# Kernel optimization log

Measured on AMD Instinct MI355X. Metric: run time of the kernel, lower is better.

Reference implementation:

```python
import jax, jax.numpy as jnp
import numpy as np

NEG_BIG = -1e9


def setup_inputs() -> dict:
    key = jax.random.key(0)
    ks = jax.random.split(key, 6)
    B, Tq, Tv, D, A = 4, 256, 1024, 512, 128
    inputs = jax.random.normal(ks[0], (B, Tv, D), dtype=jnp.float32)
    context = jax.random.normal(ks[1], (B, Tq, D), dtype=jnp.float32)
    mask = jnp.ones((B, Tv), dtype=jnp.int32)  # 1 = valid position
    scale = 1.0 / np.sqrt(D)
    Wk = jax.random.normal(ks[2], (D, A), dtype=jnp.float32) * scale
    bk = jnp.zeros((A,), dtype=jnp.float32)
    Wq = jax.random.normal(ks[3], (D, A), dtype=jnp.float32) * scale
    bq = jnp.zeros((A,), dtype=jnp.float32)
    attn_v = jax.random.normal(ks[4], (A,), dtype=jnp.float32) * (1.0 / np.sqrt(A))
    return {"inputs": inputs, "context": context, "mask": mask,
            "Wk": Wk, "bk": bk, "Wq": Wq, "bq": bq, "attn_v": attn_v}


def reference(inputs, context, mask, Wk, bk, Wq, bq, attn_v):
    # inputs: [B,Tv,D] (keys/values), context: [B,Tq,D] (queries)
    k = jnp.einsum('bvd,da->bva', inputs, Wk) + bk        # [B,Tv,A]
    q = jnp.einsum('bqd,da->bqa', context, Wq) + bq       # [B,Tq,A]
    # additive (Bahdanau) score: sum_a v_a * tanh(q + k)
    t = jnp.tanh(q[:, :, None, :] + k[:, None, :, :])     # [B,Tq,Tv,A]
    scores = jnp.einsum('bqva,a->bqv', t, attn_v)         # [B,Tq,Tv]
    neg = (1.0 - mask.astype(jnp.float32))[:, None, :] * NEG_BIG
    scores = scores + neg
    attn = jax.nn.softmax(scores, axis=-1)                # [B,Tq,Tv]
    return jnp.einsum('bqv,bvd->bqd', attn, inputs)       # [B,Tq,D]
```

## Files before the change

### kernel.cpp

```cpp
#include <hip/hip_runtime.h>
#include <math.h>

#define B   4
#define TQ  256
#define TV  1024
#define D   512
#define A   128

#define LOG2E     1.4426950408889634f
#define TWO_LOG2E 2.8853900817779268f
#define NEG_BIG_F (-1e9f)

#define QBLK (B * TQ / 8)
#define KBLK (B * TV / 8)

__global__ __launch_bounds__(256, 4) void proj_exp_kernel(
    const float* __restrict__ ctx, const float* __restrict__ inp,
    const float* __restrict__ Wq, const float* __restrict__ bq,
    const float* __restrict__ Wk, const float* __restrict__ bk,
    float* __restrict__ Eq, float* __restrict__ EkT) {
  __shared__ float xs[8][D];
  __shared__ float ps[8][4][A];
  __shared__ float es[A][9];

  bool isQ = blockIdx.x < QBLK;
  const float* X; const float* W; const float* bias; int r0;
  if (isQ) { X = ctx; W = Wq; bias = bq; r0 = blockIdx.x * 8; }
  else     { X = inp; W = Wk; bias = bk; r0 = (blockIdx.x - QBLK) * 8; }

  int tid = threadIdx.x;

  {
    const float4* Xv = (const float4*)(X + (size_t)r0 * D);
    float4* xsv = (float4*)&xs[0][0];
    for (int i = tid; i < 8 * D / 4; i += 256) xsv[i] = Xv[i];
  }
  __syncthreads();

  int aq = (tid & 31) * 4;
  int h  = tid >> 5;
  float4 acc[8];
#pragma unroll
  for (int j = 0; j < 8; ++j) acc[j] = make_float4(0.f, 0.f, 0.f, 0.f);

  int dbase = h * 64;
#pragma unroll 2
  for (int dd = 0; dd < 64; dd += 4) {
    int d = dbase + dd;
    float4 w0 = *(const float4*)(W + (size_t)(d + 0) * A + aq);
    float4 w1 = *(const float4*)(W + (size_t)(d + 1) * A + aq);
    float4 w2 = *(const float4*)(W + (size_t)(d + 2) * A + aq);
    float4 w3 = *(const float4*)(W + (size_t)(d + 3) * A + aq);
#pragma unroll
    for (int j = 0; j < 8; ++j) {
      float4 x = *(const float4*)&xs[j][d];
      acc[j].x = fmaf(x.x, w0.x, acc[j].x);
      acc[j].y = fmaf(x.x, w0.y, acc[j].y);
      acc[j].z = fmaf(x.x, w0.z, acc[j].z);
      acc[j].w = fmaf(x.x, w0.w, acc[j].w);
      acc[j].x = fmaf(x.y, w1.x, acc[j].x);
      acc[j].y = fmaf(x.y, w1.y, acc[j].y);
      acc[j].z = fmaf(x.y, w1.z, acc[j].z);
      acc[j].w = fmaf(x.y, w1.w, acc[j].w);
      acc[j].x = fmaf(x.z, w2.x, acc[j].x);
      acc[j].y = fmaf(x.z, w2.y, acc[j].y);
      acc[j].z = fmaf(x.z, w2.z, acc[j].z);
      acc[j].w = fmaf(x.z, w2.w, acc[j].w);
      acc[j].x = fmaf(x.w, w3.x, acc[j].x);
      acc[j].y = fmaf(x.w, w3.y, acc[j].y);
      acc[j].z = fmaf(x.w, w3.z, acc[j].z);
      acc[j].w = fmaf(x.w, w3.w, acc[j].w);
    }
  }

#pragma unroll
  for (int j = 0; j < 8; ++j) {
    acc[j].x += __shfl_down(acc[j].x, 32, 64);
    acc[j].y += __shfl_down(acc[j].y, 32, 64);
    acc[j].z += __shfl_down(acc[j].z, 32, 64);
    acc[j].w += __shfl_down(acc[j].w, 32, 64);
  }
  int g = tid >> 6;
  if ((tid & 63) < 32) {
#pragma unroll
    for (int j = 0; j < 8; ++j)
      *(float4*)&ps[j][g][aq] = acc[j];
  }
  __syncthreads();

  int j  = tid >> 5;
  int a4 = (tid & 31) * 4;
  float4 p0 = *(const float4*)&ps[j][0][a4];
  float4 p1 = *(const float4*)&ps[j][1][a4];
  float4 p2 = *(const float4*)&ps[j][2][a4];
  float4 p3 = *(const float4*)&ps[j][3][a4];
  float4 bz = *(const float4*)(bias + a4);
  float4 ev;
  ev.x = __builtin_amdgcn_exp2f((((p0.x + p1.x) + (p2.x + p3.x)) + bz.x) * TWO_LOG2E);
  ev.y = __builtin_amdgcn_exp2f((((p0.y + p1.y) + (p2.y + p3.y)) + bz.y) * TWO_LOG2E);
  ev.z = __builtin_amdgcn_exp2f((((p0.z + p1.z) + (p2.z + p3.z)) + bz.z) * TWO_LOG2E);
  ev.w = __builtin_amdgcn_exp2f((((p0.w + p1.w) + (p2.w + p3.w)) + bz.w) * TWO_LOG2E);

  if (isQ) {
    *(float4*)(Eq + (size_t)(r0 + j) * A + a4) = ev;
  } else {
    es[a4 + 0][j] = ev.x;
    es[a4 + 1][j] = ev.y;
    es[a4 + 2][j] = ev.z;
    es[a4 + 3][j] = ev.w;
    __syncthreads();
    int b  = r0 >> 10;
    int v0 = r0 & (TV - 1);
    for (int i = tid; i < A * 8; i += 256) {
      int aa = i >> 3, jj = i & 7;
      EkT[((size_t)b * A + aa) * TV + v0 + jj] = es[aa][jj];
    }
  }
}

__global__ __launch_bounds__(256, 4) void score_softmax_kernel(
    const float* __restrict__ Eq, const float* __restrict__ EkT,
    const float* __restrict__ attn_v, const int* __restrict__ mask,
    float* __restrict__ attn) {
  __shared__ float redA[4], redB[4];
  __shared__ float bc[4];

  int tid = threadIdx.x;
  int v0  = (tid & 63) * 4 + (tid >> 6) * 256;
  int r0  = blockIdx.x * 2;
  int b   = r0 >> 8;

  const float* eqA = Eq + (size_t)r0 * A;
  const float* eqB = eqA + A;

  float sumV = 0.f;
#pragma unroll 16
  for (int i = 0; i < A; ++i) sumV += attn_v[i];

  const float* ekb = EkT + (size_t)b * A * TV + v0;
  float4 tA = make_float4(0.f, 0.f, 0.f, 0.f);
  float4 tB = make_float4(0.f, 0.f, 0.f, 0.f);

  float4 e0 = *(const float4*)(ekb);
  float4 e1 = *(const float4*)(ekb + (size_t)TV);
#pragma unroll 4
  for (int i = 0; i < A; ++i) {
    float4 en;
    if (i < A - 2) en = *(const float4*)(ekb + (size_t)(i + 2) * TV);
    float av = attn_v[i];
    float qa = eqA[i];
    float qb = eqB[i];
    tA.x = fmaf(av, __builtin_amdgcn_rcpf(fmaf(e0.x, qa, 1.f)), tA.x);
    tA.y = fmaf(av, __builtin_amdgcn_rcpf(fmaf(e0.y, qa, 1.f)), tA.y);
    tA.z = fmaf(av, __builtin_amdgcn_rcpf(fmaf(e0.z, qa, 1.f)), tA.z);
    tA.w = fmaf(av, __builtin_amdgcn_rcpf(fmaf(e0.w, qa, 1.f)), tA.w);
    tB.x = fmaf(av, __builtin_amdgcn_rcpf(fmaf(e0.x, qb, 1.f)), tB.x);
    tB.y = fmaf(av, __builtin_amdgcn_rcpf(fmaf(e0.y, qb, 1.f)), tB.y);
    tB.z = fmaf(av, __builtin_amdgcn_rcpf(fmaf(e0.z, qb, 1.f)), tB.z);
    tB.w = fmaf(av, __builtin_amdgcn_rcpf(fmaf(e0.w, qb, 1.f)), tB.w);
    e0 = e1;
    e1 = en;
  }

  int4 mk = *(const int4*)(mask + b * TV + v0);
  float4 sA, sB;
  sA.x = sumV - 2.f * tA.x + (1.f - (float)mk.x) * NEG_BIG_F;
  sA.y = sumV - 2.f * tA.y + (1.f - (float)mk.y) * NEG_BIG_F;
  sA.z = sumV - 2.f * tA.z + (1.f - (float)mk.z) * NEG_BIG_F;
  sA.w = sumV - 2.f * tA.w + (1.f - (float)mk.w) * NEG_BIG_F;
  sB.x = sumV - 2.f * tB.x + (1.f - (float)mk.x) * NEG_BIG_F;
  sB.y = sumV - 2.f * tB.y + (1.f - (float)mk.y) * NEG_BIG_F;
  sB.z = sumV - 2.f * tB.z + (1.f - (float)mk.z) * NEG_BIG_F;
  sB.w = sumV - 2.f * tB.w + (1.f - (float)mk.w) * NEG_BIG_F;

  float mA = fmaxf(fmaxf(sA.x, sA.y), fmaxf(sA.z, sA.w));
  float mB = fmaxf(fmaxf(sB.x, sB.y), fmaxf(sB.z, sB.w));
  for (int off = 32; off > 0; off >>= 1) {
    mA = fmaxf(mA, __shfl_down(mA, off, 64));
    mB = fmaxf(mB, __shfl_down(mB, off, 64));
  }
  int w = tid >> 6;
  if ((tid & 63) == 0) { redA[w] = mA; redB[w] = mB; }
  __syncthreads();
  if (tid == 0) {
    bc[0] = fmaxf(fmaxf(redA[0], redA[1]), fmaxf(redA[2], redA[3]));
    bc[1] = fmaxf(fmaxf(redB[0], redB[1]), fmaxf(redB[2], redB[3]));
  }
  __syncthreads();
  float MA = bc[0], MB = bc[1];

  float4 eAv, eBv;
  eAv.x = __builtin_amdgcn_exp2f((sA.x - MA) * LOG2E);
  eAv.y = __builtin_amdgcn_exp2f((sA.y - MA) * LOG2E);
  eAv.z = __builtin_amdgcn_exp2f((sA.z - MA) * LOG2E);
  eAv.w = __builtin_amdgcn_exp2f((sA.w - MA) * LOG2E);
  eBv.x = __builtin_amdgcn_exp2f((sB.x - MB) * LOG2E);
  eBv.y = __builtin_amdgcn_exp2f((sB.y - MB) * LOG2E);
  eBv.z = __builtin_amdgcn_exp2f((sB.z - MB) * LOG2E);
  eBv.w = __builtin_amdgcn_exp2f((sB.w - MB) * LOG2E);
  float lA = (eAv.x + eAv.y) + (eAv.z + eAv.w);
  float lB = (eBv.x + eBv.y) + (eBv.z + eBv.w);
  for (int off = 32; off > 0; off >>= 1) {
    lA += __shfl_down(lA, off, 64);
    lB += __shfl_down(lB, off, 64);
  }
  __syncthreads();
  if ((tid & 63) == 0) { redA[w] = lA; redB[w] = lB; }
  __syncthreads();
  if (tid == 0) {
    bc[2] = (redA[0] + redA[1]) + (redA[2] + redA[3]);
    bc[3] = (redB[0] + redB[1]) + (redB[2] + redB[3]);
  }
  __syncthreads();
  float iA = 1.f / bc[2];
  float iB = 1.f / bc[3];

  float4 oA = make_float4(eAv.x * iA, eAv.y * iA, eAv.z * iA, eAv.w * iA);
  float4 oB = make_float4(eBv.x * iB, eBv.y * iB, eBv.z * iB, eBv.w * iB);
  *(float4*)(attn + (size_t)r0 * TV + v0)       = oA;
  *(float4*)(attn + (size_t)(r0 + 1) * TV + v0) = oB;
}

__global__ __launch_bounds__(512, 4) void pv_kernel(
    const float* __restrict__ attn, const float* __restrict__ X,
    float* __restrict__ out) {
  __shared__ float lds[8 * 1024];
  int dt = blockIdx.x;
  int q0 = blockIdx.y * 8;
  int b  = q0 >> 8;
  int tid  = threadIdx.x;
  int w    = tid >> 6;
  int lane = tid & 63;
  int col  = lane & 31;
  int qh   = lane >> 5;
  int d0 = dt * 128 + col * 4;

  {
    const float4* src = (const float4*)(attn + (size_t)q0 * TV);
    float4* dst = (float4*)lds;
    for (int i = tid; i < 8 * 256; i += 512) dst[i] = src[i];
  }
  __syncthreads();

  float4 acc[4];
#pragma unroll
  for (int j = 0; j < 4; ++j) acc[j] = make_float4(0.f, 0.f, 0.f, 0.f);

  int vbase = w * 128;
  const float* Xb = X + ((size_t)b * TV + vbase) * D + d0;
  const float* arow = &lds[(qh * 4) * 1024 + vbase];

  float4 xc0 = *(const float4*)(Xb + (size_t)0 * D);
  float4 xc1 = *(const float4*)(Xb + (size_t)1 * D);
  float4 xc2 = *(const float4*)(Xb + (size_t)2 * D);
  float4 xc3 = *(const float4*)(Xb + (size_t)3 * D);

  for (int vi = 0; vi < 128; vi += 4) {
    float4 xn0, xn1, xn2, xn3;
    if (vi < 124) {
      const float* Xn = Xb + (size_t)(vi + 4) * D;
      xn0 = *(const float4*)(Xn + (size_t)0 * D);
      xn1 = *(const float4*)(Xn + (size_t)1 * D);
      xn2 = *(const float4*)(Xn + (size_t)2 * D);
      xn3 = *(const float4*)(Xn + (size_t)3 * D);
    }
#pragma unroll
    for (int j = 0; j < 4; ++j) {
      float4 av = *(const float4*)(arow + j * 1024 + vi);
      acc[j].x = fmaf(av.x, xc0.x, acc[j].x);
      acc[j].y = fmaf(av.x, xc0.y, acc[j].y);
      acc[j].z = fmaf(av.x, xc0.z, acc[j].z);
      acc[j].w = fmaf(av.x, xc0.w, acc[j].w);
      acc[j].x = fmaf(av.y, xc1.x, acc[j].x);
      acc[j].y = fmaf(av.y, xc1.y, acc[j].y);
      acc[j].z = fmaf(av.y, xc1.z, acc[j].z);
      acc[j].w = fmaf(av.y, xc1.w, acc[j].w);
      acc[j].x = fmaf(av.z, xc2.x, acc[j].x);
      acc[j].y = fmaf(av.z, xc2.y, acc[j].y);
      acc[j].z = fmaf(av.z, xc2.z, acc[j].z);
      acc[j].w = fmaf(av.z, xc2.w, acc[j].w);
      acc[j].x = fmaf(av.w, xc3.x, acc[j].x);
      acc[j].y = fmaf(av.w, xc3.y, acc[j].y);
      acc[j].z = fmaf(av.w, xc3.z, acc[j].z);
      acc[j].w = fmaf(av.w, xc3.w, acc[j].w);
    }
    xc0 = xn0; xc1 = xn1; xc2 = xn2; xc3 = xn3;
  }

  __syncthreads();

  {
    float4* pat = (float4*)lds + (size_t)w * 256;
#pragma unroll
    for (int j = 0; j < 4; ++j)
      pat[(qh * 4 + j) * 32 + col] = acc[j];
  }
  __syncthreads();

  if (tid < 256) {
    int row = tid >> 5;
    int c   = tid & 31;
    const float4* p = (const float4*)lds + tid;
    float4 r = p[0];
#pragma unroll
    for (int i = 1; i < 8; ++i) {
      float4 t = p[(size_t)i * 256];
      r.x += t.x; r.y += t.y; r.z += t.z; r.w += t.w;
    }
    *(float4*)(out + (size_t)(q0 + row) * D + dt * 128 + c * 4) = r;
  }
}

extern "C" void kernel_launch(void* const* d_in, const int* in_sizes, int n_in,
                              void* d_out, int out_size, void* d_ws, size_t ws_size,
                              hipStream_t stream) {
  const float* inputs  = (const float*)d_in[0];
  const float* context = (const float*)d_in[1];
  const int*   mask    = (const int*)d_in[2];
  const float* Wk      = (const float*)d_in[3];
  const float* bk      = (const float*)d_in[4];
  const float* Wq      = (const float*)d_in[5];
  const float* bq      = (const float*)d_in[6];
  const float* attn_v  = (const float*)d_in[7];
  float* out = (float*)d_out;

  float* Eq   = (float*)d_ws;
  float* EkT  = Eq + B * TQ * A;
  float* attn = EkT + (size_t)B * A * TV;

  proj_exp_kernel<<<QBLK + KBLK, 256, 0, stream>>>(context, inputs, Wq, bq,
                                                   Wk, bk, Eq, EkT);
  score_softmax_kernel<<<B * TQ / 2, 256, 0, stream>>>(Eq, EkT, attn_v, mask,
                                                       attn);
  pv_kernel<<<dim3(4, 128), 512, 0, stream>>>(attn, inputs, out);
}
```

Before: 138.9 us.

## Drop LDS staging in projection and double query rows per PV block

Result: slower. 142.5 us (+2.6%).

```diff
diff --git a/kernel.cpp b/kernel.cpp
--- a/kernel.cpp
+++ b/kernel.cpp
@@ -19,7 +19,6 @@
     const float* __restrict__ Wq, const float* __restrict__ bq,
     const float* __restrict__ Wk, const float* __restrict__ bk,
     float* __restrict__ Eq, float* __restrict__ EkT) {
-  __shared__ float xs[8][D];
   __shared__ float ps[8][4][A];
   __shared__ float es[A][9];
 
@@ -29,63 +28,43 @@
   else     { X = inp; W = Wk; bias = bk; r0 = (blockIdx.x - QBLK) * 8; }
 
   int tid = threadIdx.x;
-
-  {
-    const float4* Xv = (const float4*)(X + (size_t)r0 * D);
-    float4* xsv = (float4*)&xs[0][0];
-    for (int i = tid; i < 8 * D / 4; i += 256) xsv[i] = Xv[i];
-  }
-  __syncthreads();
-
-  int aq = (tid & 31) * 4;
-  int h  = tid >> 5;
-  float4 acc[8];
-#pragma unroll
-  for (int j = 0; j < 8; ++j) acc[j] = make_float4(0.f, 0.f, 0.f, 0.f);
-
-  int dbase = h * 64;
+  int ap = (tid & 63) * 2;
+  int g  = tid >> 6;
+
+  int dbase = __builtin_amdgcn_readfirstlane(g * 128);
+  const float* Xr = X + (size_t)r0 * D + dbase;
+  const float* Wd = W + (size_t)dbase * A + ap;
+
+  float2 acc[8];
+#pragma unroll
+  for (int j = 0; j < 8; ++j) acc[j] = make_float2(0.f, 0.f);
+
 #pragma unroll 2
-  for (int dd = 0; dd < 64; dd += 4) {
-    int d = dbase + dd;
-    float4 w0 = *(const float4*)(W + (size_t)(d + 0) * A + aq);
-    float4 w1 = *(const float4*)(W + (size_t)(d + 1) * A + aq);
-    float4 w2 = *(const float4*)(W + (size_t)(d + 2) * A + aq);
-    float4 w3 = *(const float4*)(W + (size_t)(d + 3) * A + aq);
+  for (int dd = 0; dd < 128; dd += 4) {
+    float2 w0 = *(const float2*)(Wd + (size_t)(dd + 0) * A);
+    float2 w1 = *(const float2*)(Wd + (size_t)(dd + 1) * A);
+    float2 w2 = *(const float2*)(Wd + (size_t)(dd + 2) * A);
+    float2 w3 = *(const float2*)(Wd + (size_t)(dd + 3) * A);
+    float4 x[8];
+#pragma unroll
+    for (int j = 0; j < 8; ++j)
+      x[j] = *(const float4*)(Xr + (size_t)j * D + dd);
 #pragma unroll
     for (int j = 0; j < 8; ++j) {
-      float4 x = *(const float4*)&xs[j][d];
-      acc[j].x = fmaf(x.x, w0.x, acc[j].x);
-      acc[j].y = fmaf(x.x, w0.y, acc[j].y);
-      acc[j].z = fmaf(x.x, w0.z, acc[j].z);
-      acc[j].w = fmaf(x.x, w0.w, acc[j].w);
-      acc[j].x = fmaf(x.y, w1.x, acc[j].x);
-      acc[j].y = fmaf(x.y, w1.y, acc[j].y);
-      acc[j].z = fmaf(x.y, w1.z, acc[j].z);
-      acc[j].w = fmaf(x.y, w1.w, acc[j].w);
-      acc[j].x = fmaf(x.z, w2.x, acc[j].x);
-      acc[j].y = fmaf(x.z, w2.y, acc[j].y);
-      acc[j].z = fmaf(x.z, w2.z, acc[j].z);
-      acc[j].w = fmaf(x.z, w2.w, acc[j].w);
-      acc[j].x = fmaf(x.w, w3.x, acc[j].x);
-      acc[j].y = fmaf(x.w, w3.y, acc[j].y);
-      acc[j].z = fmaf(x.w, w3.z, acc[j].z);
-      acc[j].w = fmaf(x.w, w3.w, acc[j].w);
-    }
-  }
-
-#pragma unroll
-  for (int j = 0; j < 8; ++j) {
-    acc[j].x += __shfl_down(acc[j].x, 32, 64);
-    acc[j].y += __shfl_down(acc[j].y, 32, 64);
-    acc[j].z += __shfl_down(acc[j].z, 32, 64);
-    acc[j].w += __shfl_down(acc[j].w, 32, 64);
-  }
-  int g = tid >> 6;
-  if ((tid & 63) < 32) {
-#pragma unroll
-    for (int j = 0; j < 8; ++j)
-      *(float4*)&ps[j][g][aq] = acc[j];
-  }
+      acc[j].x = fmaf(x[j].x, w0.x, acc[j].x);
+      acc[j].y = fmaf(x[j].x, w0.y, acc[j].y);
+      acc[j].x = fmaf(x[j].y, w1.x, acc[j].x);
+      acc[j].y = fmaf(x[j].y, w1.y, acc[j].y);
+      acc[j].x = fmaf(x[j].z, w2.x, acc[j].x);
+      acc[j].y = fmaf(x[j].z, w2.y, acc[j].y);
+      acc[j].x = fmaf(x[j].w, w3.x, acc[j].x);
+      acc[j].y = fmaf(x[j].w, w3.y, acc[j].y);
+    }
+  }
+
+#pragma unroll
+  for (int j = 0; j < 8; ++j)
+    *(float2*)&ps[j][g][ap] = acc[j];
   __syncthreads();
 
   int j  = tid >> 5;
@@ -221,12 +200,12 @@
   *(float4*)(attn + (size_t)(r0 + 1) * TV + v0) = oB;
 }
 
-__global__ __launch_bounds__(512, 4) void pv_kernel(
+__global__ __launch_bounds__(512, 2) void pv_kernel(
     const float* __restrict__ attn, const float* __restrict__ X,
     float* __restrict__ out) {
-  __shared__ float lds[8 * 1024];
+  __shared__ float lds[16 * 1024];
   int dt = blockIdx.x;
-  int q0 = blockIdx.y * 8;
+  int q0 = blockIdx.y * 16;
   int b  = q0 >> 8;
   int tid  = threadIdx.x;
   int w    = tid >> 6;
@@ -238,17 +217,17 @@
   {
     const float4* src = (const float4*)(attn + (size_t)q0 * TV);
     float4* dst = (float4*)lds;
-    for (int i = tid; i < 8 * 256; i += 512) dst[i] = src[i];
-  }
-  __syncthreads();
-
-  float4 acc[4];
-#pragma unroll
-  for (int j = 0; j < 4; ++j) acc[j] = make_float4(0.f, 0.f, 0.f, 0.f);
+    for (int i = tid; i < 16 * 256; i += 512) dst[i] = src[i];
+  }
+  __syncthreads();
+
+  float4 acc[8];
+#pragma unroll
+  for (int j = 0; j < 8; ++j) acc[j] = make_float4(0.f, 0.f, 0.f, 0.f);
 
   int vbase = w * 128;
   const float* Xb = X + ((size_t)b * TV + vbase) * D + d0;
-  const float* arow = &lds[(qh * 4) * 1024 + vbase];
+  const float* arow = &lds[(qh * 8) * 1024 + vbase];
 
   float4 xc0 = *(const float4*)(Xb + (size_t)0 * D);
   float4 xc1 = *(const float4*)(Xb + (size_t)1 * D);
@@ -265,7 +244,7 @@
       xn3 = *(const float4*)(Xn + (size_t)3 * D);
     }
 #pragma unroll
-    for (int j = 0; j < 4; ++j) {
+    for (int j = 0; j < 8; ++j) {
       float4 av = *(const float4*)(arow + j * 1024 + vi);
       acc[j].x = fmaf(av.x, xc0.x, acc[j].x);
       acc[j].y = fmaf(av.x, xc0.y, acc[j].y);
@@ -290,21 +269,21 @@
   __syncthreads();
 
   {
-    float4* pat = (float4*)lds + (size_t)w * 256;
-#pragma unroll
-    for (int j = 0; j < 4; ++j)
-      pat[(qh * 4 + j) * 32 + col] = acc[j];
-  }
-  __syncthreads();
-
-  if (tid < 256) {
+    float4* pat = (float4*)lds + (size_t)w * 512;
+#pragma unroll
+    for (int j = 0; j < 8; ++j)
+      pat[(qh * 8 + j) * 32 + col] = acc[j];
+  }
+  __syncthreads();
+
+  {
     int row = tid >> 5;
     int c   = tid & 31;
     const float4* p = (const float4*)lds + tid;
     float4 r = p[0];
 #pragma unroll
     for (int i = 1; i < 8; ++i) {
-      float4 t = p[(size_t)i * 256];
+      float4 t = p[(size_t)i * 512];
       r.x += t.x; r.y += t.y; r.z += t.z; r.w += t.w;
     }
     *(float4*)(out + (size_t)(q0 + row) * D + dt * 128 + c * 4) = r;
@@ -332,5 +311,5 @@
                                                    Wk, bk, Eq, EkT);
   score_softmax_kernel<<<B * TQ / 2, 256, 0, stream>>>(Eq, EkT, attn_v, mask,
                                                        attn);
-  pv_kernel<<<dim3(4, 128), 512, 0, stream>>>(attn, inputs, out);
+  pv_kernel<<<dim3(4, 64), 512, 0, stream>>>(attn, inputs, out);
 }
```
